# Kernel tuning notes

Hardware: AMD Instinct MI355X
Metric: run time of the kernel (lower is better)

## Reference

```python
import jax, jax.numpy as jnp
import numpy as np

HIDDEN = 256
NUM_REL = 6
NUM_BASES = 30
N_NODES = 50000
N_EDGES = 800000


def rgcn_gate_layer(x, src, dst, etype, basis, att, root, bias, gate_w, gate_b):
    # Basis-decomposed relation weights: W_r = sum_b att[r,b] * basis[b]
    N = x.shape[0]
    W = jnp.einsum('rb,bio->rio', att, basis)           # [R, d, d]
    # Transform all nodes under every relation (cheaper than per-edge matmul
    # since N*R < E), then gather the per-edge message.
    xw = jnp.einsum('nd,rde->rne', x, W)                # [R, N, d]
    msg = xw[etype, src]                                # [E, d]
    # Scalar sigmoid gate per edge message
    g = jax.nn.sigmoid(msg @ gate_w + gate_b)           # [E, 1]
    gated = g * msg
    # Mean aggregation over incoming edges per destination node
    agg = jax.ops.segment_sum(gated, dst, num_segments=N)
    deg = jax.ops.segment_sum(jnp.ones((src.shape[0], 1), x.dtype), dst,
                              num_segments=N)
    agg = agg / jnp.maximum(deg, 1.0)
    return agg + x @ root + bias


def setup_inputs() -> dict:
    key = jax.random.key(0)
    ks = jax.random.split(key, 16)
    d = HIDDEN
    inp = {
        'x': jax.random.normal(ks[0], (N_NODES, d), jnp.float32),
        'edge_src': jax.random.randint(ks[1], (N_EDGES,), 0, N_NODES, jnp.int32),
        'edge_dst': jax.random.randint(ks[2], (N_EDGES,), 0, N_NODES, jnp.int32),
        'edge_type': jax.random.randint(ks[3], (N_EDGES,), 0, NUM_REL, jnp.int32),
    }
    def glorot(k, shape):
        fan = shape[-2] + shape[-1]
        return jax.random.uniform(k, shape, jnp.float32,
                                  -np.sqrt(6.0 / fan), np.sqrt(6.0 / fan))
    for li, off in ((1, 4), (2, 10)):
        inp[f'basis{li}'] = glorot(ks[off + 0], (NUM_BASES, d, d))
        inp[f'att{li}'] = glorot(ks[off + 1], (NUM_REL, NUM_BASES))
        inp[f'root{li}'] = glorot(ks[off + 2], (d, d))
        inp[f'bias{li}'] = jnp.zeros((d,), jnp.float32)
        inp[f'gate_w{li}'] = glorot(ks[off + 3], (d, 1))
        inp[f'gate_b{li}'] = jnp.zeros((1,), jnp.float32)
    return inp


def reference(x, edge_src, edge_dst, edge_type,
              basis1, att1, root1, bias1, gate_w1, gate_b1,
              basis2, att2, root2, bias2, gate_w2, gate_b2):
    h = jax.nn.relu(rgcn_gate_layer(x, edge_src, edge_dst, edge_type,
                                    basis1, att1, root1, bias1,
                                    gate_w1, gate_b1))
    out = rgcn_gate_layer(h, edge_src, edge_dst, edge_type,
                          basis2, att2, root2, bias2, gate_w2, gate_b2)
    return out
```

## Files before the change

### kernel.cpp

```cpp
#include <hip/hip_runtime.h>
#include <cmath>

#define HIDDEN 256
#define NUM_REL 6
#define KA 1536
#define KB 1792
#define NK 56
#define NKA 48
#define CTSTRIDE 28672

typedef float f32x4_t __attribute__((ext_vector_type(4)));
typedef short bf16x8_t __attribute__((ext_vector_type(8)));

__device__ __forceinline__ float bf2f(ushort u) {
  return __uint_as_float(((uint)u) << 16);
}
__device__ __forceinline__ ushort f2bf(float f) {
  uint u = __float_as_uint(f);
  u += 0x7FFFu + ((u >> 16) & 1u);
  return (ushort)(u >> 16);
}

__global__ __launch_bounds__(256) void prep_weights(
    const float* __restrict__ att, const float* __restrict__ basis,
    const float* __restrict__ root, const float* __restrict__ gw,
    ushort* __restrict__ BTf, float* __restrict__ gatevec) {
  const int d = blockIdx.x, r = blockIdx.y, o = threadIdx.x;
  float v;
  if (r < 6) {
    float s = 0.f;
#pragma unroll
    for (int b = 0; b < 30; ++b)
      s += att[r * 30 + b] * basis[(size_t)b * 65536 + d * 256 + o];
    v = s;
  } else {
    v = root[d * 256 + o];
  }
  const int gk = r * 256 + d;
  BTf[(size_t)(o >> 4) * CTSTRIDE + (gk >> 3) * 128 + (o & 15) * 8 +
      (gk & 7)] = f2bf(v);
  if (r < 6) {
    float t = v * gw[o];
#pragma unroll
    for (int off = 32; off; off >>= 1) t += __shfl_xor(t, off);
    __shared__ float sums[4];
    if ((o & 63) == 0) sums[o >> 6] = t;
    __syncthreads();
    if (o == 0) gatevec[r * 256 + d] = sums[0] + sums[1] + sums[2] + sums[3];
  }
}

__global__ __launch_bounds__(256) void gdot_kernel(
    const void* __restrict__ xin, int xIsF32, ushort* __restrict__ xbOut,
    const float* __restrict__ gatevec, const float* __restrict__ gate_b,
    float* __restrict__ G, int N) {
  const int wave = (blockIdx.x * blockDim.x + threadIdx.x) >> 6;
  if (wave >= N) return;
  const int l = threadIdx.x & 63;
  float x0, x1, x2, x3;
  if (xIsF32) {
    float4 xv = ((const float4*)xin)[(size_t)wave * 64 + l];
    x0 = xv.x; x1 = xv.y; x2 = xv.z; x3 = xv.w;
    ushort4 o;
    o.x = f2bf(x0); o.y = f2bf(x1); o.z = f2bf(x2); o.w = f2bf(x3);
    ((ushort4*)xbOut)[(size_t)wave * 64 + l] = o;
  } else {
    ushort4 xv = ((const ushort4*)xin)[(size_t)wave * 64 + l];
    x0 = bf2f(xv.x); x1 = bf2f(xv.y); x2 = bf2f(xv.z); x3 = bf2f(xv.w);
  }
  float out = 0.f;
#pragma unroll
  for (int r = 0; r < NUM_REL; ++r) {
    float4 gv = ((const float4*)(gatevec + r * 256))[l];
    float d = x0 * gv.x + x1 * gv.y + x2 * gv.z + x3 * gv.w;
#pragma unroll
    for (int off = 32; off; off >>= 1) d += __shfl_xor(d, off);
    if (l == r) out = d;
  }
  if (l < NUM_REL) {
    const float gb = gate_b[0];
    G[(size_t)l * N + wave] = 1.f / (1.f + __expf(-(out + gb)));
  }
}

#define ACCUM(rj, gj, vj)                                                  \
  do {                                                                    \
    const float fx = (gj)*bf2f((vj).x), fy = (gj)*bf2f((vj).y);           \
    const float fz = (gj)*bf2f((vj).z), fw = (gj)*bf2f((vj).w);           \
    switch (rj) {                                                         \
      case 0: a0x += fx; a0y += fy; a0z += fz; a0w += fw; break;          \
      case 1: a1x += fx; a1y += fy; a1z += fz; a1w += fw; break;          \
      case 2: a2x += fx; a2y += fy; a2z += fz; a2w += fw; break;          \
      case 3: a3x += fx; a3y += fy; a3z += fz; a3w += fw; break;          \
      case 4: a4x += fx; a4y += fy; a4z += fz; a4w += fw; break;          \
      default: a5x += fx; a5y += fy; a5z += fz; a5w += fw; break;         \
    }                                                                     \
  } while (0)

#define RELOF(ei) ((ei >= b1) + (ei >= b2) + (ei >= b3) + (ei >= b4) + (ei >= b5))

__global__ __launch_bounds__(256) void edge_agg(
    const ushort* __restrict__ xb, const float* __restrict__ G,
    const int* __restrict__ rp8, const int* __restrict__ src_s,
    ushort* __restrict__ A, int N) {
  const int n = (blockIdx.x * blockDim.x + threadIdx.x) >> 6;
  if (n >= N) return;
  const int l = threadIdx.x & 63;
  const int b0 = rp8[n * 8 + 0], b1 = rp8[n * 8 + 1], b2 = rp8[n * 8 + 2];
  const int b3 = rp8[n * 8 + 3], b4 = rp8[n * 8 + 4], b5 = rp8[n * 8 + 5];
  const int b6 = rp8[n * 8 + 6];

  float a0x = 0, a0y = 0, a0z = 0, a0w = 0, a1x = 0, a1y = 0, a1z = 0, a1w = 0;
  float a2x = 0, a2y = 0, a2z = 0, a2w = 0, a3x = 0, a3y = 0, a3z = 0, a3w = 0;
  float a4x = 0, a4y = 0, a4z = 0, a4w = 0, a5x = 0, a5y = 0, a5z = 0, a5w = 0;

  int e = b0;
  for (; e + 7 < b6; e += 8) {
    const int s0 = src_s[e + 0], s1 = src_s[e + 1];
    const int s2 = src_s[e + 2], s3 = src_s[e + 3];
    const int s4 = src_s[e + 4], s5 = src_s[e + 5];
    const int s6 = src_s[e + 6], s7 = src_s[e + 7];
    const ushort4 v0 = ((const ushort4*)(xb + (size_t)s0 * 256))[l];
    const ushort4 v1 = ((const ushort4*)(xb + (size_t)s1 * 256))[l];
    const ushort4 v2 = ((const ushort4*)(xb + (size_t)s2 * 256))[l];
    const ushort4 v3 = ((const ushort4*)(xb + (size_t)s3 * 256))[l];
    const ushort4 v4 = ((const ushort4*)(xb + (size_t)s4 * 256))[l];
    const ushort4 v5 = ((const ushort4*)(xb + (size_t)s5 * 256))[l];
    const ushort4 v6 = ((const ushort4*)(xb + (size_t)s6 * 256))[l];
    const ushort4 v7 = ((const ushort4*)(xb + (size_t)s7 * 256))[l];
    const int r0 = RELOF(e + 0), r1 = RELOF(e + 1), r2 = RELOF(e + 2),
              r3 = RELOF(e + 3), r4 = RELOF(e + 4), r5 = RELOF(e + 5),
              r6 = RELOF(e + 6), r7 = RELOF(e + 7);
    const float g0 = G[(size_t)r0 * N + s0], g1 = G[(size_t)r1 * N + s1];
    const float g2 = G[(size_t)r2 * N + s2], g3 = G[(size_t)r3 * N + s3];
    const float g4 = G[(size_t)r4 * N + s4], g5 = G[(size_t)r5 * N + s5];
    const float g6 = G[(size_t)r6 * N + s6], g7 = G[(size_t)r7 * N + s7];
    ACCUM(r0, g0, v0); ACCUM(r1, g1, v1); ACCUM(r2, g2, v2); ACCUM(r3, g3, v3);
    ACCUM(r4, g4, v4); ACCUM(r5, g5, v5); ACCUM(r6, g6, v6); ACCUM(r7, g7, v7);
  }
  for (; e < b6; ++e) {
    const int s0 = src_s[e];
    const ushort4 v0 = ((const ushort4*)(xb + (size_t)s0 * 256))[l];
    const int r0 = RELOF(e);
    const float g0 = G[(size_t)r0 * N + s0];
    ACCUM(r0, g0, v0);
  }

  const float inv = 1.f / fmaxf((float)(b6 - b0), 1.f);
  ushort* Arow = A + (size_t)n * KA;
  ushort4 o;
  o.x = f2bf(a0x * inv); o.y = f2bf(a0y * inv); o.z = f2bf(a0z * inv); o.w = f2bf(a0w * inv);
  ((ushort4*)(Arow + 0 * 256))[l] = o;
  o.x = f2bf(a1x * inv); o.y = f2bf(a1y * inv); o.z = f2bf(a1z * inv); o.w = f2bf(a1w * inv);
  ((ushort4*)(Arow + 1 * 256))[l] = o;
  o.x = f2bf(a2x * inv); o.y = f2bf(a2y * inv); o.z = f2bf(a2z * inv); o.w = f2bf(a2w * inv);
  ((ushort4*)(Arow + 2 * 256))[l] = o;
  o.x = f2bf(a3x * inv); o.y = f2bf(a3y * inv); o.z = f2bf(a3z * inv); o.w = f2bf(a3w * inv);
  ((ushort4*)(Arow + 3 * 256))[l] = o;
  o.x = f2bf(a4x * inv); o.y = f2bf(a4y * inv); o.z = f2bf(a4z * inv); o.w = f2bf(a4w * inv);
  ((ushort4*)(Arow + 4 * 256))[l] = o;
  o.x = f2bf(a5x * inv); o.y = f2bf(a5y * inv); o.z = f2bf(a5z * inv); o.w = f2bf(a5w * inv);
  ((ushort4*)(Arow + 5 * 256))[l] = o;
}

__global__ __launch_bounds__(256) void gemm_fused(
    const ushort* __restrict__ A, const ushort* __restrict__ xb,
    const ushort* __restrict__ BTf, const float* __restrict__ bias,
    void* __restrict__ outPtr, int M, int mode) {
  __shared__ ushort As[3][64 * 32];
  const int row0 = blockIdx.x * 64;
  const int tid = threadIdx.x;
  const int w = tid >> 6, l = tid & 63;

  const int srow = tid >> 2;
  const int ssc = (tid & 3) ^ (srow & 3) ^ ((srow >> 2) & 3);
  const int ga = min(row0 + srow, M - 1);
  const ushort* gpA = A + (size_t)ga * KA + ssc * 8;
  const ushort* gpX = xb + (size_t)ga * 256 + ssc * 8;

  const ushort* Bb =
      BTf + (size_t)(w * 4) * CTSTRIDE + (l >> 4) * 128 + (l & 15) * 8;

  f32x4_t acc[4][4] = {};

  auto stage = [&](int k, int buf) {
    const ushort* gp = (k < NKA) ? (gpA + k * 32) : (gpX + (k * 32 - KA));
    __builtin_amdgcn_global_load_lds(
        (const __attribute__((address_space(1))) void*)gp,
        (__attribute__((address_space(3))) void*)(&As[buf][tid * 8]), 16, 0, 0);
  };

  auto compute = [&](int buf, const bf16x8_t* b) {
    bf16x8_t a[4];
#pragma unroll
    for (int m = 0; m < 4; ++m) {
      const int rr = m * 16 + (l & 15);
      const int c = (l >> 4) ^ (rr & 3) ^ ((rr >> 2) & 3);
      a[m] = *(const bf16x8_t*)(&As[buf][rr * 32 + c * 8]);
    }
#pragma unroll
    for (int m = 0; m < 4; ++m)
#pragma unroll
      for (int n = 0; n < 4; ++n)
        acc[m][n] = __builtin_amdgcn_mfma_f32_16x16x32_bf16(a[m], b[n],
                                                            acc[m][n], 0, 0, 0);
  };

  bf16x8_t bE[4], bO[4];
  stage(0, 0);
  stage(1, 1);
#pragma unroll
  for (int n = 0; n < 4; ++n)
    bE[n] = *(const bf16x8_t*)(Bb + (size_t)n * CTSTRIDE);

  for (int k = 0; k < NK; k += 2) {
    asm volatile("s_waitcnt vmcnt(5)" ::: "memory");
    __builtin_amdgcn_s_barrier();
#pragma unroll
    for (int n = 0; n < 4; ++n)
      bO[n] = *(const bf16x8_t*)(Bb + (size_t)n * CTSTRIDE + (k + 1) * 512);
    if (k + 2 < NK) stage(k + 2, (k + 2) % 3);
    compute(k % 3, bE);

    asm volatile("s_waitcnt vmcnt(5)" ::: "memory");
    __builtin_amdgcn_s_barrier();
    if (k + 2 < NK) {
#pragma unroll
      for (int n = 0; n < 4; ++n)
        bE[n] = *(const bf16x8_t*)(Bb + (size_t)n * CTSTRIDE + (k + 2) * 512);
    }
    if (k + 3 < NK) stage(k + 3, (k + 3) % 3);
    compute((k + 1) % 3, bO);
  }

  const int rbase = row0 + (l >> 4) * 4;
  const int cbase = w * 64 + (l & 15);
#pragma unroll
  for (int n = 0; n < 4; ++n) {
    const int col = cbase + n * 16;
    const float bv = bias[col];
#pragma unroll
    for (int m = 0; m < 4; ++m)
#pragma unroll
      for (int i = 0; i < 4; ++i) {
        const int row = rbase + m * 16 + i;
        if (row < M) {
          float v = acc[m][n][i] + bv;
          if (mode == 0) {
            v = fmaxf(v, 0.f);
            ((ushort*)outPtr)[(size_t)row * 256 + col] = f2bf(v);
          } else {
            ((float*)outPtr)[(size_t)row * 256 + col] = v;
          }
        }
      }
  }
}

__global__ void hist_kernel(const int* __restrict__ dst,
                            const int* __restrict__ ety,
                            int* __restrict__ cnt, int E) {
  int stride = gridDim.x * blockDim.x;
  for (int e = blockIdx.x * blockDim.x + threadIdx.x; e < E; e += stride)
    atomicAdd(&cnt[dst[e] * 8 + ety[e]], 1);
}

__global__ void scan_reduce(const int* __restrict__ cnt,
                            int* __restrict__ blockSums, int n) {
  __shared__ int sd[256];
  int base = blockIdx.x * 1024;
  int t = threadIdx.x;
  int s = 0;
#pragma unroll
  for (int i = 0; i < 4; ++i) {
    int idx = base + t * 4 + i;
    s += (idx < n) ? cnt[idx] : 0;
  }
  sd[t] = s; __syncthreads();
  for (int off = 128; off; off >>= 1) {
    if (t < off) sd[t] += sd[t + off];
    __syncthreads();
  }
  if (t == 0) blockSums[blockIdx.x] = sd[0];
}

__global__ void scan_offsets(int* __restrict__ blockSums, int nb) {
  __shared__ int sd[512];
  const int t = threadIdx.x;
  const int v = (t < nb) ? blockSums[t] : 0;
  sd[t] = v; __syncthreads();
  for (int off = 1; off < 512; off <<= 1) {
    int u = (t >= off) ? sd[t - off] : 0;
    __syncthreads();
    sd[t] += u;
    __syncthreads();
  }
  if (t < nb) blockSums[t] = sd[t] - v;
}

__global__ void scan_write(const int* __restrict__ cnt,
                           const int* __restrict__ blockSums,
                           int* __restrict__ row_ptr, int* __restrict__ cursor,
                           int n) {
  __shared__ int sd[256];
  int base = blockIdx.x * 1024;
  int t = threadIdx.x;
  int v[4]; int s = 0;
#pragma unroll
  for (int i = 0; i < 4; ++i) {
    int idx = base + t * 4 + i;
    v[i] = (idx < n) ? cnt[idx] : 0;
    s += v[i];
  }
  sd[t] = s; __syncthreads();
  for (int off = 1; off < 256; off <<= 1) {
    int val = (t >= off) ? sd[t - off] : 0;
    __syncthreads();
    sd[t] += val;
    __syncthreads();
  }
  int excl = blockSums[blockIdx.x] + sd[t] - s;
  for (int i = 0; i < 4; ++i) {
    int idx = base + t * 4 + i;
    if (idx < n) {
      row_ptr[idx] = excl;
      cursor[idx] = excl;
      excl += v[i];
      if (idx == n - 1) row_ptr[n] = excl;
    }
  }
}

__global__ void scatter_kernel(const int* __restrict__ src,
                               const int* __restrict__ dst,
                               const int* __restrict__ ety,
                               int* __restrict__ cursor,
                               int* __restrict__ src_s, int E) {
  int stride = gridDim.x * blockDim.x;
  for (int e = blockIdx.x * blockDim.x + threadIdx.x; e < E; e += stride) {
    int bin = dst[e] * 8 + ety[e];
    int pos = atomicAdd(&cursor[bin], 1);
    src_s[pos] = src[e];
  }
}

static inline size_t align16(size_t x) { return (x + 15) & ~(size_t)15; }

extern "C" void kernel_launch(void* const* d_in, const int* in_sizes, int n_in,
                              void* d_out, int out_size, void* d_ws,
                              size_t ws_size, hipStream_t stream) {
  const float* x    = (const float*)d_in[0];
  const int*   src  = (const int*)d_in[1];
  const int*   dst  = (const int*)d_in[2];
  const int*   ety  = (const int*)d_in[3];

  const int N   = in_sizes[0] / HIDDEN;
  const int E   = in_sizes[1];
  const int RN2 = N * 8;

  char* p = (char*)d_ws;
  ushort* BTf    = (ushort*)p; p += align16(((size_t)16 * CTSTRIDE + 4096) * 2);
  float* gatevec = (float*)p;  p += align16((size_t)NUM_REL * 256 * 4);
  float* G       = (float*)p;  p += align16((size_t)NUM_REL * N * 4);
  ushort* xb0    = (ushort*)p; p += align16((size_t)N * HIDDEN * 2);
  ushort* xb1    = (ushort*)p; p += align16((size_t)N * HIDDEN * 2);
  int* cnt       = (int*)p;    p += align16((size_t)RN2 * 4);
  int* cursor    = (int*)p;    p += align16((size_t)RN2 * 4);
  int* row_ptr   = (int*)p;    p += align16((size_t)(RN2 + 1) * 4);
  int* blockSums = (int*)p;    p += 2048;
  int* src_s     = (int*)p;    p += align16((size_t)E * 4);
  ushort* A      = (ushort*)p;

  const int scanBlocks = (RN2 + 1023) / 1024;

  hipMemsetAsync(cnt, 0, (size_t)RN2 * sizeof(int), stream);
  hist_kernel<<<2048, 256, 0, stream>>>(dst, ety, cnt, E);
  scan_reduce<<<scanBlocks, 256, 0, stream>>>(cnt, blockSums, RN2);
  scan_offsets<<<1, 512, 0, stream>>>(blockSums, scanBlocks);
  scan_write<<<scanBlocks, 256, 0, stream>>>(cnt, blockSums, row_ptr, cursor,
                                             RN2);
  scatter_kernel<<<2048, 256, 0, stream>>>(src, dst, ety, cursor, src_s, E);

  const int nodeBlocks = (N * 64 + 255) / 256;
  const int gemmGrid = (N + 63) / 64;

  for (int layer = 0; layer < 2; ++layer) {
    const float* bas  = (const float*)d_in[layer ? 10 : 4];
    const float* att  = (const float*)d_in[layer ? 11 : 5];
    const float* root = (const float*)d_in[layer ? 12 : 6];
    const float* bias = (const float*)d_in[layer ? 13 : 7];
    const float* gw   = (const float*)d_in[layer ? 14 : 8];
    const float* gb   = (const float*)d_in[layer ? 15 : 9];
    const ushort* xb  = layer ? xb1 : xb0;
    void* outp = layer ? d_out : (void*)xb1;
    const int mode = layer ? 1 : 0;

    prep_weights<<<dim3(256, 7), 256, 0, stream>>>(att, bas, root, gw, BTf,
                                                   gatevec);
    gdot_kernel<<<nodeBlocks, 256, 0, stream>>>(
        layer ? (const void*)xb1 : (const void*)x, layer ? 0 : 1, xb0,
        gatevec, gb, G, N);
    edge_agg<<<nodeBlocks, 256, 0, stream>>>(xb, G, row_ptr, src_s, A, N);
    gemm_fused<<<gemmGrid, 256, 0, stream>>>(A, xb, BTf, bias, outp, N, mode);
  }
}
```

Measured before the change: 512.5 us.

## Split GEMM output columns across two blocks and record per-edge rank to drop scatter atomics

The fused GEMM now gives each block half of the 256 output columns (128), which doubles the grid and halves the accumulators and B loads per wave. This raises occupancy and block count for the roughly 782-row-tile problem, at the cost of loading each A tile twice. Separately, the histogram pass stores each edge's atomic return value as its rank within its bin. The scatter pass then computes the position as row_ptr plus rank instead of doing a second atomic, and the cursor array goes away. This removes one round of contended atomics in exchange for an extra E-sized int array write and read.

After: 494.0 us. 3.6% less time.

```diff
diff --git a/kernel.cpp b/kernel.cpp
--- a/kernel.cpp
+++ b/kernel.cpp
@@ -168,7 +168,9 @@
     const ushort* __restrict__ BTf, const float* __restrict__ bias,
     void* __restrict__ outPtr, int M, int mode) {
   __shared__ ushort As[3][64 * 32];
-  const int row0 = blockIdx.x * 64;
+  const int bid = blockIdx.x;
+  const int row0 = (bid >> 1) * 64;
+  const int colh = bid & 1;
   const int tid = threadIdx.x;
   const int w = tid >> 6, l = tid & 63;
 
@@ -178,10 +180,10 @@
   const ushort* gpA = A + (size_t)ga * KA + ssc * 8;
   const ushort* gpX = xb + (size_t)ga * 256 + ssc * 8;
 
-  const ushort* Bb =
-      BTf + (size_t)(w * 4) * CTSTRIDE + (l >> 4) * 128 + (l & 15) * 8;
-
-  f32x4_t acc[4][4] = {};
+  const ushort* Bb = BTf + (size_t)(colh * 8 + w * 2) * CTSTRIDE +
+                     (l >> 4) * 128 + (l & 15) * 8;
+
+  f32x4_t acc[4][2] = {};
 
   auto stage = [&](int k, int buf) {
     const ushort* gp = (k < NKA) ? (gpA + k * 32) : (gpX + (k * 32 - KA));
@@ -201,32 +203,32 @@
 #pragma unroll
     for (int m = 0; m < 4; ++m)
 #pragma unroll
-      for (int n = 0; n < 4; ++n)
+      for (int n = 0; n < 2; ++n)
         acc[m][n] = __builtin_amdgcn_mfma_f32_16x16x32_bf16(a[m], b[n],
                                                             acc[m][n], 0, 0, 0);
   };
 
-  bf16x8_t bE[4], bO[4];
+  bf16x8_t bE[2], bO[2];
   stage(0, 0);
   stage(1, 1);
 #pragma unroll
-  for (int n = 0; n < 4; ++n)
+  for (int n = 0; n < 2; ++n)
     bE[n] = *(const bf16x8_t*)(Bb + (size_t)n * CTSTRIDE);
 
   for (int k = 0; k < NK; k += 2) {
-    asm volatile("s_waitcnt vmcnt(5)" ::: "memory");
+    asm volatile("s_waitcnt vmcnt(3)" ::: "memory");
     __builtin_amdgcn_s_barrier();
 #pragma unroll
-    for (int n = 0; n < 4; ++n)
+    for (int n = 0; n < 2; ++n)
       bO[n] = *(const bf16x8_t*)(Bb + (size_t)n * CTSTRIDE + (k + 1) * 512);
     if (k + 2 < NK) stage(k + 2, (k + 2) % 3);
     compute(k % 3, bE);
 
-    asm volatile("s_waitcnt vmcnt(5)" ::: "memory");
+    asm volatile("s_waitcnt vmcnt(3)" ::: "memory");
     __builtin_amdgcn_s_barrier();
     if (k + 2 < NK) {
 #pragma unroll
-      for (int n = 0; n < 4; ++n)
+      for (int n = 0; n < 2; ++n)
         bE[n] = *(const bf16x8_t*)(Bb + (size_t)n * CTSTRIDE + (k + 2) * 512);
     }
     if (k + 3 < NK) stage(k + 3, (k + 3) % 3);
@@ -234,9 +236,9 @@
   }
 
   const int rbase = row0 + (l >> 4) * 4;
-  const int cbase = w * 64 + (l & 15);
-#pragma unroll
-  for (int n = 0; n < 4; ++n) {
+  const int cbase = colh * 128 + w * 32 + (l & 15);
+#pragma unroll
+  for (int n = 0; n < 2; ++n) {
     const int col = cbase + n * 16;
     const float bv = bias[col];
 #pragma unroll
@@ -259,10 +261,11 @@
 
 __global__ void hist_kernel(const int* __restrict__ dst,
                             const int* __restrict__ ety,
-                            int* __restrict__ cnt, int E) {
+                            int* __restrict__ cnt, int* __restrict__ erank,
+                            int E) {
   int stride = gridDim.x * blockDim.x;
   for (int e = blockIdx.x * blockDim.x + threadIdx.x; e < E; e += stride)
-    atomicAdd(&cnt[dst[e] * 8 + ety[e]], 1);
+    erank[e] = atomicAdd(&cnt[dst[e] * 8 + ety[e]], 1);
 }
 
 __global__ void scan_reduce(const int* __restrict__ cnt,
@@ -300,8 +303,7 @@
 
 __global__ void scan_write(const int* __restrict__ cnt,
                            const int* __restrict__ blockSums,
-                           int* __restrict__ row_ptr, int* __restrict__ cursor,
-                           int n) {
+                           int* __restrict__ row_ptr, int n) {
   __shared__ int sd[256];
   int base = blockIdx.x * 1024;
   int t = threadIdx.x;
@@ -324,7 +326,6 @@
     int idx = base + t * 4 + i;
     if (idx < n) {
       row_ptr[idx] = excl;
-      cursor[idx] = excl;
       excl += v[i];
       if (idx == n - 1) row_ptr[n] = excl;
     }
@@ -334,13 +335,13 @@
 __global__ void scatter_kernel(const int* __restrict__ src,
                                const int* __restrict__ dst,
                                const int* __restrict__ ety,
-                               int* __restrict__ cursor,
+                               const int* __restrict__ row_ptr,
+                               const int* __restrict__ erank,
                                int* __restrict__ src_s, int E) {
   int stride = gridDim.x * blockDim.x;
   for (int e = blockIdx.x * blockDim.x + threadIdx.x; e < E; e += stride) {
     int bin = dst[e] * 8 + ety[e];
-    int pos = atomicAdd(&cursor[bin], 1);
-    src_s[pos] = src[e];
+    src_s[row_ptr[bin] + erank[e]] = src[e];
   }
 }
 
@@ -365,7 +366,7 @@
   ushort* xb0    = (ushort*)p; p += align16((size_t)N * HIDDEN * 2);
   ushort* xb1    = (ushort*)p; p += align16((size_t)N * HIDDEN * 2);
   int* cnt       = (int*)p;    p += align16((size_t)RN2 * 4);
-  int* cursor    = (int*)p;    p += align16((size_t)RN2 * 4);
+  int* erank     = (int*)p;    p += align16((size_t)E * 4);
   int* row_ptr   = (int*)p;    p += align16((size_t)(RN2 + 1) * 4);
   int* blockSums = (int*)p;    p += 2048;
   int* src_s     = (int*)p;    p += align16((size_t)E * 4);
@@ -374,15 +375,15 @@
   const int scanBlocks = (RN2 + 1023) / 1024;
 
   hipMemsetAsync(cnt, 0, (size_t)RN2 * sizeof(int), stream);
-  hist_kernel<<<2048, 256, 0, stream>>>(dst, ety, cnt, E);
+  hist_kernel<<<2048, 256, 0, stream>>>(dst, ety, cnt, erank, E);
   scan_reduce<<<scanBlocks, 256, 0, stream>>>(cnt, blockSums, RN2);
   scan_offsets<<<1, 512, 0, stream>>>(blockSums, scanBlocks);
-  scan_write<<<scanBlocks, 256, 0, stream>>>(cnt, blockSums, row_ptr, cursor,
-                                             RN2);
-  scatter_kernel<<<2048, 256, 0, stream>>>(src, dst, ety, cursor, src_s, E);
+  scan_write<<<scanBlocks, 256, 0, stream>>>(cnt, blockSums, row_ptr, RN2);
+  scatter_kernel<<<2048, 256, 0, stream>>>(src, dst, ety, row_ptr, erank,
+                                           src_s, E);
 
   const int nodeBlocks = (N * 64 + 255) / 256;
-  const int gemmGrid = (N + 63) / 64;
+  const int gemmGrid = 2 * ((N + 63) / 64);
 
   for (int layer = 0; layer < 2; ++layer) {
     const float* bas  = (const float*)d_in[layer ? 10 : 4];
```

## Stream per-relation accumulators in edge_agg and precompute edge ranks in histogram

Applied to the files above, without the earlier changes.

The edge aggregation kernel now keeps a single float4 accumulator and writes each relation's mean row out as soon as the sorted edge list moves past that relation. This replaces 24 per-relation accumulators and a switch-based dispatch, cutting register pressure and branching. Separately, the histogram kernel records each edge's atomic rank, so the scatter kernel can compute positions directly from row_ptr without a second round of atomics on a cursor array. The cost is an extra E-sized rank array in workspace and data-dependent flush loops inside the unrolled edge loop.

After: 496.5 us. -3.1%, faster.

```diff
diff --git a/kernel.cpp b/kernel.cpp
--- a/kernel.cpp
+++ b/kernel.cpp
@@ -83,20 +83,6 @@
   }
 }
 
-#define ACCUM(rj, gj, vj)                                                  \
-  do {                                                                    \
-    const float fx = (gj)*bf2f((vj).x), fy = (gj)*bf2f((vj).y);           \
-    const float fz = (gj)*bf2f((vj).z), fw = (gj)*bf2f((vj).w);           \
-    switch (rj) {                                                         \
-      case 0: a0x += fx; a0y += fy; a0z += fz; a0w += fw; break;          \
-      case 1: a1x += fx; a1y += fy; a1z += fz; a1w += fw; break;          \
-      case 2: a2x += fx; a2y += fy; a2z += fz; a2w += fw; break;          \
-      case 3: a3x += fx; a3y += fy; a3z += fz; a3w += fw; break;          \
-      case 4: a4x += fx; a4y += fy; a4z += fz; a4w += fw; break;          \
-      default: a5x += fx; a5y += fy; a5z += fz; a5w += fw; break;         \
-    }                                                                     \
-  } while (0)
-
 #define RELOF(ei) ((ei >= b1) + (ei >= b2) + (ei >= b3) + (ei >= b4) + (ei >= b5))
 
 __global__ __launch_bounds__(256) void edge_agg(
@@ -110,9 +96,25 @@
   const int b3 = rp8[n * 8 + 3], b4 = rp8[n * 8 + 4], b5 = rp8[n * 8 + 5];
   const int b6 = rp8[n * 8 + 6];
 
-  float a0x = 0, a0y = 0, a0z = 0, a0w = 0, a1x = 0, a1y = 0, a1z = 0, a1w = 0;
-  float a2x = 0, a2y = 0, a2z = 0, a2w = 0, a3x = 0, a3y = 0, a3z = 0, a3w = 0;
-  float a4x = 0, a4y = 0, a4z = 0, a4w = 0, a5x = 0, a5y = 0, a5z = 0, a5w = 0;
+  const float inv = 1.f / fmaxf((float)(b6 - b0), 1.f);
+  ushort* Arow = A + (size_t)n * KA;
+
+  float ax = 0.f, ay = 0.f, az = 0.f, aw = 0.f;
+  int cur = 0;
+
+#define FLUSH_TO(rj)                                                     \
+  while (cur < (rj)) {                                                   \
+    ushort4 o;                                                           \
+    o.x = f2bf(ax * inv); o.y = f2bf(ay * inv);                          \
+    o.z = f2bf(az * inv); o.w = f2bf(aw * inv);                          \
+    ((ushort4*)(Arow + cur * 256))[l] = o;                               \
+    ax = ay = az = aw = 0.f;                                             \
+    ++cur;                                                               \
+  }
+
+#define ACC1(gj, vj)                                                     \
+  ax += (gj)*bf2f((vj).x); ay += (gj)*bf2f((vj).y);                      \
+  az += (gj)*bf2f((vj).z); aw += (gj)*bf2f((vj).w);
 
   int e = b0;
   for (; e + 7 < b6; e += 8) {
@@ -135,32 +137,26 @@
     const float g2 = G[(size_t)r2 * N + s2], g3 = G[(size_t)r3 * N + s3];
     const float g4 = G[(size_t)r4 * N + s4], g5 = G[(size_t)r5 * N + s5];
     const float g6 = G[(size_t)r6 * N + s6], g7 = G[(size_t)r7 * N + s7];
-    ACCUM(r0, g0, v0); ACCUM(r1, g1, v1); ACCUM(r2, g2, v2); ACCUM(r3, g3, v3);
-    ACCUM(r4, g4, v4); ACCUM(r5, g5, v5); ACCUM(r6, g6, v6); ACCUM(r7, g7, v7);
+    FLUSH_TO(r0); ACC1(g0, v0);
+    FLUSH_TO(r1); ACC1(g1, v1);
+    FLUSH_TO(r2); ACC1(g2, v2);
+    FLUSH_TO(r3); ACC1(g3, v3);
+    FLUSH_TO(r4); ACC1(g4, v4);
+    FLUSH_TO(r5); ACC1(g5, v5);
+    FLUSH_TO(r6); ACC1(g6, v6);
+    FLUSH_TO(r7); ACC1(g7, v7);
   }
   for (; e < b6; ++e) {
     const int s0 = src_s[e];
     const ushort4 v0 = ((const ushort4*)(xb + (size_t)s0 * 256))[l];
     const int r0 = RELOF(e);
     const float g0 = G[(size_t)r0 * N + s0];
-    ACCUM(r0, g0, v0);
-  }
-
-  const float inv = 1.f / fmaxf((float)(b6 - b0), 1.f);
-  ushort* Arow = A + (size_t)n * KA;
-  ushort4 o;
-  o.x = f2bf(a0x * inv); o.y = f2bf(a0y * inv); o.z = f2bf(a0z * inv); o.w = f2bf(a0w * inv);
-  ((ushort4*)(Arow + 0 * 256))[l] = o;
-  o.x = f2bf(a1x * inv); o.y = f2bf(a1y * inv); o.z = f2bf(a1z * inv); o.w = f2bf(a1w * inv);
-  ((ushort4*)(Arow + 1 * 256))[l] = o;
-  o.x = f2bf(a2x * inv); o.y = f2bf(a2y * inv); o.z = f2bf(a2z * inv); o.w = f2bf(a2w * inv);
-  ((ushort4*)(Arow + 2 * 256))[l] = o;
-  o.x = f2bf(a3x * inv); o.y = f2bf(a3y * inv); o.z = f2bf(a3z * inv); o.w = f2bf(a3w * inv);
-  ((ushort4*)(Arow + 3 * 256))[l] = o;
-  o.x = f2bf(a4x * inv); o.y = f2bf(a4y * inv); o.z = f2bf(a4z * inv); o.w = f2bf(a4w * inv);
-  ((ushort4*)(Arow + 4 * 256))[l] = o;
-  o.x = f2bf(a5x * inv); o.y = f2bf(a5y * inv); o.z = f2bf(a5z * inv); o.w = f2bf(a5w * inv);
-  ((ushort4*)(Arow + 5 * 256))[l] = o;
+    FLUSH_TO(r0); ACC1(g0, v0);
+  }
+  FLUSH_TO(6);
+
+#undef FLUSH_TO
+#undef ACC1
 }
 
 __global__ __launch_bounds__(256) void gemm_fused(
@@ -259,10 +255,11 @@
 
 __global__ void hist_kernel(const int* __restrict__ dst,
                             const int* __restrict__ ety,
-                            int* __restrict__ cnt, int E) {
+                            int* __restrict__ cnt, int* __restrict__ erank,
+                            int E) {
   int stride = gridDim.x * blockDim.x;
   for (int e = blockIdx.x * blockDim.x + threadIdx.x; e < E; e += stride)
-    atomicAdd(&cnt[dst[e] * 8 + ety[e]], 1);
+    erank[e] = atomicAdd(&cnt[dst[e] * 8 + ety[e]], 1);
 }
 
 __global__ void scan_reduce(const int* __restrict__ cnt,
@@ -300,8 +297,7 @@
 
 __global__ void scan_write(const int* __restrict__ cnt,
                            const int* __restrict__ blockSums,
-                           int* __restrict__ row_ptr, int* __restrict__ cursor,
-                           int n) {
+                           int* __restrict__ row_ptr, int n) {
   __shared__ int sd[256];
   int base = blockIdx.x * 1024;
   int t = threadIdx.x;
@@ -324,7 +320,6 @@
     int idx = base + t * 4 + i;
     if (idx < n) {
       row_ptr[idx] = excl;
-      cursor[idx] = excl;
       excl += v[i];
       if (idx == n - 1) row_ptr[n] = excl;
     }
@@ -334,13 +329,13 @@
 __global__ void scatter_kernel(const int* __restrict__ src,
                                const int* __restrict__ dst,
                                const int* __restrict__ ety,
-                               int* __restrict__ cursor,
+                               const int* __restrict__ row_ptr,
+                               const int* __restrict__ erank,
                                int* __restrict__ src_s, int E) {
   int stride = gridDim.x * blockDim.x;
   for (int e = blockIdx.x * blockDim.x + threadIdx.x; e < E; e += stride) {
     int bin = dst[e] * 8 + ety[e];
-    int pos = atomicAdd(&cursor[bin], 1);
-    src_s[pos] = src[e];
+    src_s[row_ptr[bin] + erank[e]] = src[e];
   }
 }
 
@@ -365,7 +360,7 @@
   ushort* xb0    = (ushort*)p; p += align16((size_t)N * HIDDEN * 2);
   ushort* xb1    = (ushort*)p; p += align16((size_t)N * HIDDEN * 2);
   int* cnt       = (int*)p;    p += align16((size_t)RN2 * 4);
-  int* cursor    = (int*)p;    p += align16((size_t)RN2 * 4);
+  int* erank     = (int*)p;    p += align16((size_t)E * 4);
   int* row_ptr   = (int*)p;    p += align16((size_t)(RN2 + 1) * 4);
   int* blockSums = (int*)p;    p += 2048;
   int* src_s     = (int*)p;    p += align16((size_t)E * 4);
@@ -374,12 +369,12 @@
   const int scanBlocks = (RN2 + 1023) / 1024;
 
   hipMemsetAsync(cnt, 0, (size_t)RN2 * sizeof(int), stream);
-  hist_kernel<<<2048, 256, 0, stream>>>(dst, ety, cnt, E);
+  hist_kernel<<<2048, 256, 0, stream>>>(dst, ety, cnt, erank, E);
   scan_reduce<<<scanBlocks, 256, 0, stream>>>(cnt, blockSums, RN2);
   scan_offsets<<<1, 512, 0, stream>>>(blockSums, scanBlocks);
-  scan_write<<<scanBlocks, 256, 0, stream>>>(cnt, blockSums, row_ptr, cursor,
-                                             RN2);
-  scatter_kernel<<<2048, 256, 0, stream>>>(src, dst, ety, cursor, src_s, E);
+  scan_write<<<scanBlocks, 256, 0, stream>>>(cnt, blockSums, row_ptr, RN2);
+  scatter_kernel<<<2048, 256, 0, stream>>>(src, dst, ety, row_ptr, erank,
+                                           src_s, E);
 
   const int nodeBlocks = (N * 64 + 255) / 256;
   const int gemmGrid = (N + 63) / 64;
```
